# Kernel tuning notes

Measured on AMD Instinct MI355X. Metric: run time of the kernel, lower is better.

Reference implementation:

```python
import jax, jax.numpy as jnp
import numpy as np

# Fixed model constants from setParams()
TAU_W, TAU_N, TAU_R = 1.5e6, 6.0e5, 6.0e4
TAU_E, TAU_G, TAU_A = 2.5e4, 1.0e4, 1.0e4
F_W_MAX, F_N_MAX, F_R_MAX = 6.5, 5.0, 5.0
ALPHA_W, ALPHA_N, ALPHA_R = 0.5, 0.175, 0.13
BETA_W, BETA_R = -0.4, -0.9
GAMMA_E, GAMMA_G, GAMMA_A = 5.0, 4.0, 2.0
H_MAX, THETA_W = 1.0, 2.0
TAU_HW, TAU_HS = 3.483e7, 3.06e7
KAPPA = 1.5
A_RK = (0.5, 0.5, 1.0, 1.0)

T, B = 10000, 512


def setup_inputs() -> dict:
    key = jax.random.key(0)
    noise = 0.05 * jax.random.normal(key, (T, B), dtype=jnp.float32)
    return {
        "noise_input": noise,
        "g_RRe": jnp.float32(1.3),
        "g_RWe": jnp.float32(1.6),
        "g_WNi": jnp.float32(-2.0),
        "g_WRi": jnp.float32(-4.0),
        "g_NRi": jnp.float32(-1.3),
        "g_NWi": jnp.float32(-1.68),
    }


def _heaviside(x):
    # smooth heaviside: sigmoid with steepness 5
    return jax.nn.sigmoid(5.0 * x)


def reference(noise_input, g_RRe, g_RWe, g_WNi, g_WRi, g_NRi, g_NWi):
    b = noise_input.shape[1]
    dt = noise_input.dtype
    init = (
        jnp.full((b,), 6.0, dt),    # f_W
        jnp.full((b,), 1e-3, dt),   # f_N
        jnp.full((b,), 1e-3, dt),   # f_R
        jnp.full((b,), 0.9, dt),    # c_WXi
        jnp.full((b,), 1e-3, dt),   # c_NXi
        jnp.full((b,), 1e-3, dt),   # c_RXe
        jnp.full((b,), 0.5, dt),    # h
    )

    def step(state, noise):
        fW0, fN0, fR0, cW0, cN0, cR0, h0 = state
        # RK moment lists; index 0 is the step's initial value
        fW = [fW0]; fN = [fN0]; fR = [fR0]
        cW = [cW0]; cN = [cN0]; cR = [cR0]; hh = [h0]
        for n in range(4):
            a = A_RK[n]
            I_W = g_NWi * cN[n] + g_RWe * cR[n] + noise
            I_N = g_WNi * cW[n] + noise
            I_R = g_WRi * cW[n] + g_NRi * cN[n] + g_RRe * cR[n] + noise
            fW.append(fW[0] + a * (F_W_MAX * 0.5 * (1.0 + jnp.tanh((I_W - BETA_W) / ALPHA_W)) - fW[n]) / TAU_W)
            fN.append(fN[0] + a * (F_N_MAX * 0.5 * (1.0 + jnp.tanh((I_N + KAPPA * hh[n]) / ALPHA_N)) - fN[n]) / TAU_N)
            fR.append(fR[0] + a * (F_R_MAX * 0.5 * (1.0 + jnp.tanh((I_R - BETA_R) / ALPHA_R)) - fR[n]) / TAU_R)
            cW.append(cW[0] + a * (jnp.tanh(fW[n + 1] / GAMMA_E) - cW[n]) / TAU_E)
            cN.append(cN[0] + a * (jnp.tanh(fN[n + 1] / GAMMA_G) - cN[n]) / TAU_G)
            cR.append(cR[0] + a * (jnp.tanh(fR[n + 1] / GAMMA_A) - cR[n]) / TAU_A)
            hh.append(hh[0] + a * ((H_MAX - hh[n]) / TAU_HW * _heaviside(fW[n] - THETA_W)
                                   - hh[n] / TAU_HS * _heaviside(THETA_W - fW[n])))
        comb = lambda v: (-3.0 * v[0] + 2.0 * v[1] + 4.0 * v[2] + 2.0 * v[3] + v[4]) / 6.0
        new_state = tuple(comb(v) for v in (fW, fN, fR, cW, cN, cR, hh))
        return new_state, jnp.stack(new_state)  # [7, B]

    _, traj = jax.lax.scan(step, init, noise_input)
    return traj  # [T, 7, B]
```

## Files before the change

### kernel.cpp

```cpp
#include <hip/hip_runtime.h>

#define T_STEPS 10000
#define BATCH   512

__device__ __forceinline__ float fexp2(float x) {
#if __has_builtin(__builtin_amdgcn_exp2f)
  return __builtin_amdgcn_exp2f(x);
#else
  return exp2f(x);
#endif
}

__device__ __forceinline__ float frcp(float x) {
#if __has_builtin(__builtin_amdgcn_rcpf)
  return __builtin_amdgcn_rcpf(x);
#else
  return 1.0f / x;
#endif
}

#define PIN(x) asm volatile("" : "+v"(x))

template <int CTRL>
__device__ __forceinline__ float qperm(float v) {
  int i = __builtin_bit_cast(int, v);
#if __has_builtin(__builtin_amdgcn_mov_dpp)
  int r = __builtin_amdgcn_mov_dpp(i, CTRL, 0xF, 0xF, true);
#else
  int r = __builtin_amdgcn_ds_swizzle(i, 0x8000 | CTRL);
#endif
  return __builtin_bit_cast(float, r);
}

__global__ __launch_bounds__(64, 1)
void sleep_rk4_kernel(const float* __restrict__ noise,
                      const float* __restrict__ pgRRe,
                      const float* __restrict__ pgRWe,
                      const float* __restrict__ pgWNi,
                      const float* __restrict__ pgWRi,
                      const float* __restrict__ pgNRi,
                      const float* __restrict__ pgNWi,
                      float* __restrict__ out)
{
  __shared__ float shm[16 * 128];

  const int tid  = (int)(blockIdx.x * 64u + threadIdx.x);
  const int b    = tid >> 2;
  const int bl   = b & 15;
  const int role = tid & 3;

  const float g_RRe = *pgRRe, g_RWe = *pgRWe, g_WNi = *pgWNi;
  const float g_WRi = *pgWRi, g_NRi = *pgNRi, g_NWi = *pgNWi;

  const float L2E = 1.4426950408889634f;
  const float LN2 = 0.6931471805599453f;

  float W1, W2, W3, NSC, BB, qa, qb, pa, pb, cs, ia, ib;
  float f0, c0;
  bool role03;

  if (role == 0) {
    const float SC = 2.0f * L2E / 0.5f;
    W1 = SC * g_NWi; W2 = SC * g_RWe; W3 = 0.0f; NSC = SC; BB = SC * 0.4f;
    qa = -1.0f / 1.5e6f; qb = 6.5f / 1.5e6f; pa = 0.0f; pb = -6.5f / 1.5e6f;
    cs = 2.0f * L2E / 5.0f; ia = -1.0f / 2.5e4f; ib = 1.0f / 2.5e4f;
    f0 = 6.0f; c0 = 0.9f; role03 = true;
  } else if (role == 1) {
    const float SC = 2.0f * L2E / 0.175f;
    W1 = SC * g_WNi; W2 = SC * 1.5f; W3 = 0.0f; NSC = SC; BB = 0.0f;
    qa = -1.0f / 6.0e5f; qb = 5.0f / 6.0e5f; pa = 0.0f; pb = -5.0f / 6.0e5f;
    cs = 2.0f * L2E / 4.0f; ia = -1.0f / 1.0e4f; ib = 1.0f / 1.0e4f;
    f0 = 1.0e-3f; c0 = 1.0e-3f; role03 = false;
  } else if (role == 2) {
    const float SC = 2.0f * L2E / 0.13f;
    W1 = SC * g_WRi; W2 = SC * g_NRi; W3 = SC * g_RRe; NSC = SC; BB = SC * 0.9f;
    qa = -1.0f / 6.0e4f; qb = 5.0f / 6.0e4f; pa = 0.0f; pb = -5.0f / 6.0e4f;
    cs = 2.0f * L2E / 2.0f; ia = -1.0f / 1.0e4f; ib = 1.0f / 1.0e4f;
    f0 = 1.0e-3f; c0 = 1.0e-3f; role03 = false;
  } else {
    W1 = 0.0f; W2 = -5.0f * L2E; W3 = 0.0f; NSC = 0.0f; BB = 10.0f * L2E;
    qa = -1.0f / 3.06e7f; qb = 0.0f;
    pa = (1.0f / 3.06e7f - 1.0f / 3.483e7f);
    pb = 1.0f / 3.483e7f;
    cs = 0.0f; ia = 0.0f; ib = 0.0f;
    f0 = 0.5f; c0 = 0.0f; role03 = true;
  }

  const float AQAh = 0.5f * qa, AQA1 = qa;
  const float AIAh = 0.5f * ia, AIA1 = ia;
  const float IAC  = ia * cs;
  const float TIA  = 2.0f * ia;
  const float R6   = 0.16666666666666666f;

  float vF[4], vG[4];
  auto frun = [&](float f0b, float Gb, float* v) -> float {
    const float Chb = fmaf(0.5f, Gb, f0b), C1b = f0b + Gb;
    float s0 = f0b, acc = -3.0f * f0b;
    s0 = fmaf(AQAh, s0, Chb); v[0] = s0; acc = fmaf(2.0f, s0, acc);
    s0 = fmaf(AQAh, s0, Chb); v[1] = s0; acc = fmaf(4.0f, s0, acc);
    s0 = fmaf(AQA1, s0, C1b); v[2] = s0; acc = fmaf(2.0f, s0, acc);
    s0 = fmaf(AQA1, s0, C1b); v[3] = s0; acc = fmaf(1.0f, s0, acc);
    float q = acc * R6; q = fmaf(fmaf(q, -6.0f, acc), R6, q); return q;
  };
  const float KF = frun(1.0f, 0.0f, vF);
  const float KG = frun(0.0f, 1.0f, vG);

  auto crun = [&](const float* v, float c0b, float e1u, float vd1) -> float {
    const float E1h = IAC * e1u, E11 = 2.0f * IAC * e1u;
    const float Dh = c0b + 0.5f * vd1, D1 = c0b + vd1;
    float s1 = c0b, acc = -3.0f * c0b;
    s1 = fmaf(AIAh, s1, fmaf(E1h, v[0], Dh)); acc = fmaf(2.0f, s1, acc);
    s1 = fmaf(AIAh, s1, fmaf(E1h, v[1], Dh)); acc = fmaf(4.0f, s1, acc);
    s1 = fmaf(AIA1, s1, fmaf(E11, v[2], D1)); acc = fmaf(2.0f, s1, acc);
    s1 = fmaf(AIA1, s1, fmaf(E11, v[3], D1)); acc = fmaf(1.0f, s1, acc);
    float q = acc * R6; q = fmaf(fmaf(q, -6.0f, acc), R6, q); return q;
  };
  float z4[4] = {0.0f, 0.0f, 0.0f, 0.0f};
  const float KC  = crun(z4, 1.0f, 0.0f, 0.0f);
  const float LAf = crun(vF, 0.0f, 1.0f, 0.0f);
  const float LBf = crun(vG, 0.0f, 1.0f, 0.0f);
  const float KW  = crun(z4, 0.0f, 0.0f, 1.0f);

  const float KGi  = 1.0f / KG;
  const float LBfK = LBf * KGi;
  const float qbK  = qb * KG;

  float LAe, LBK, VDK, PK, tLAe, tLBK, tVDK, tPK;
  auto crefresh_compute = [&](float fcur) {
    const float zb = cs * fcur;
    const float ez = fexp2(zb);
    const float sc_ = frcp(1.0f + ez);
    const float t2 = fmaf(sc_, sc_, -sc_);
    const float e1 = LN2 * t2;
    const float vC = fmaf(-e1, zb, sc_);
    const float VD1 = fmaf(TIA, vC, ib);
    tLAe = LAf * e1; tLBK = LBfK * e1; tVDK = KW * VD1;
    tPK = fmaf(pa, fcur, pb) * KG;
  };
  crefresh_compute(f0);
  LAe = tLAe; LBK = tLBK; VDK = tVDK; PK = tPK;

  float dF = 0.0f, dC = 0.0f;
  float Gq0, Gq1, Gq2, Gq3, Gq4, Gq5, Gq6, Gq7;

  const int offA = role * 16 + bl;
  const int offB = (role + 4) * 16 + bl;

  int ldoff[7], goff[7];
  {
    const int L = (int)threadIdx.x;
    const int bb = (int)(blockIdx.x * 16u);
#pragma unroll
    for (int r = 0; r < 7; ++r) {
      const int F  = r * 64 + L;
      const int s_ = F / 28;
      const int u  = F % 28;
      const int rg = u >> 2;
      const int uu = u & 3;
      const int v  = (rg == 3) ? 6 : ((rg < 3) ? rg : rg - 1);
      ldoff[r] = s_ * 128 + u * 4;
      goff[r]  = s_ * 3584 + v * 512 + uu * 4 + bb;
    }
  }
  float* gflush = out;

  float nb0[16], nb1[16];
#pragma unroll
  for (int j = 0; j < 16; ++j) nb0[j] = noise[b + j * BATCH];

  {
    const float pubS = role03 ? f0 : c0;
    const float xAs = qperm<0x01>(c0);
    const float xBs = qperm<0x1E>(pubS);
    const float YB = fmaf(W1, xAs, fmaf(W2, xBs, fmaf(W3, c0, BB)));
    Gq0 = fmaf(PK, frcp(1.0f + fexp2(fmaf(NSC, nb0[0], YB))), qbK);
    Gq1 = fmaf(PK, frcp(1.0f + fexp2(fmaf(NSC, nb0[1], YB))), qbK);
    Gq2 = fmaf(PK, frcp(1.0f + fexp2(fmaf(NSC, nb0[2], YB))), qbK);
    Gq3 = fmaf(PK, frcp(1.0f + fexp2(fmaf(NSC, nb0[3], YB))), qbK);
    Gq4 = fmaf(PK, frcp(1.0f + fexp2(fmaf(NSC, nb0[4], YB))), qbK);
    Gq5 = fmaf(PK, frcp(1.0f + fexp2(fmaf(NSC, nb0[5], YB))), qbK);
    Gq6 = fmaf(PK, frcp(1.0f + fexp2(fmaf(NSC, nb0[6], YB))), qbK);
    Gq7 = fmaf(PK, frcp(1.0f + fexp2(fmaf(NSC, nb0[7], YB))), qbK);
  }

  auto GROUP8 = [&](int SJ, float n0, float n1, float n2, float n3,
                    float n4, float n5, float n6, float n7) {
    const float pubS = role03 ? f0 : c0;
    const float pubD = role03 ? dF : dC;
    const float xAs = qperm<0x01>(c0);
    const float xBs = qperm<0x1E>(pubS);
    const float xAd = qperm<0x01>(dC);
    const float xBd = qperm<0x1E>(pubD);
    float YB = fmaf(W3, c0, BB);
    float dY = W3 * dC;
    const float f1 = fmaf(KF, f0, Gq0);
    const float c1 = fmaf(KC, c0, fmaf(LAe, f0, fmaf(LBK, Gq0, VDK)));
    YB = fmaf(W2, xBs, YB);
    dY = fmaf(W2, xBd, dY);
    const float f2 = fmaf(KF, f1, Gq1);
    const float c2 = fmaf(KC, c1, fmaf(LAe, f1, fmaf(LBK, Gq1, VDK)));
    YB = fmaf(W1, xAs, YB);
    dY = fmaf(W1, xAd, dY);
    const float f3 = fmaf(KF, f2, Gq2);
    const float c3 = fmaf(KC, c2, fmaf(LAe, f2, fmaf(LBK, Gq2, VDK)));
    const float y0 = fmaf(NSC, n0, fmaf( 8.5f, dY, YB));
    const float y1 = fmaf(NSC, n1, fmaf( 9.5f, dY, YB));
    const float y2 = fmaf(NSC, n2, fmaf(10.5f, dY, YB));
    const float y3 = fmaf(NSC, n3, fmaf(11.5f, dY, YB));
    const float f4 = fmaf(KF, f3, Gq3);
    const float c4 = fmaf(KC, c3, fmaf(LAe, f3, fmaf(LBK, Gq3, VDK)));
    const float y4 = fmaf(NSC, n4, fmaf(12.5f, dY, YB));
    const float y5 = fmaf(NSC, n5, fmaf(13.5f, dY, YB));
    const float y6 = fmaf(NSC, n6, fmaf(14.5f, dY, YB));
    const float y7 = fmaf(NSC, n7, fmaf(15.5f, dY, YB));
    const float e0 = fexp2(y0);
    const float e1_ = fexp2(y1);
    const float f5 = fmaf(KF, f4, Gq4);
    const float c5 = fmaf(KC, c4, fmaf(LAe, f4, fmaf(LBK, Gq4, VDK)));
    const float e2 = fexp2(y2);
    const float e3 = fexp2(y3);
    const float f6 = fmaf(KF, f5, Gq5);
    const float c6 = fmaf(KC, c5, fmaf(LAe, f5, fmaf(LBK, Gq5, VDK)));
    const float e4 = fexp2(y4);
    const float e5 = fexp2(y5);
    const float f7 = fmaf(KF, f6, Gq6);
    const float c7 = fmaf(KC, c6, fmaf(LAe, f6, fmaf(LBK, Gq6, VDK)));
    const float e6 = fexp2(y6);
    const float e7 = fexp2(y7);
    const float f8 = fmaf(KF, f7, Gq7);
    const float c8 = fmaf(KC, c7, fmaf(LAe, f7, fmaf(LBK, Gq7, VDK)));
    const float r0 = frcp(1.0f + e0);
    const float r1 = frcp(1.0f + e1_);
    const float r2 = frcp(1.0f + e2);
    const float r3 = frcp(1.0f + e3);
    const float r4 = frcp(1.0f + e4);
    const float r5 = frcp(1.0f + e5);
    const float r6 = frcp(1.0f + e6);
    const float r7 = frcp(1.0f + e7);
    shm[(SJ + 0) * 128 + offA] = f1;  shm[(SJ + 0) * 128 + offB] = c1;
    shm[(SJ + 1) * 128 + offA] = f2;  shm[(SJ + 1) * 128 + offB] = c2;
    shm[(SJ + 2) * 128 + offA] = f3;  shm[(SJ + 2) * 128 + offB] = c3;
    shm[(SJ + 3) * 128 + offA] = f4;  shm[(SJ + 3) * 128 + offB] = c4;
    shm[(SJ + 4) * 128 + offA] = f5;  shm[(SJ + 4) * 128 + offB] = c5;
    shm[(SJ + 5) * 128 + offA] = f6;  shm[(SJ + 5) * 128 + offB] = c6;
    shm[(SJ + 6) * 128 + offA] = f7;  shm[(SJ + 6) * 128 + offB] = c7;
    shm[(SJ + 7) * 128 + offA] = f8;  shm[(SJ + 7) * 128 + offB] = c8;
    Gq0 = fmaf(PK, r0, qbK);
    Gq1 = fmaf(PK, r1, qbK);
    Gq2 = fmaf(PK, r2, qbK);
    Gq3 = fmaf(PK, r3, qbK);
    Gq4 = fmaf(PK, r4, qbK);
    Gq5 = fmaf(PK, r5, qbK);
    Gq6 = fmaf(PK, r6, qbK);
    Gq7 = fmaf(PK, r7, qbK);
    dF = f8 - f7; dC = c8 - c7;
    f0 = f8; c0 = c8;
  };

  int base = 0;

#define TBLOCK(nbC, nbN)                                                      \
  do {                                                                        \
    int tl = base + 16; if (tl > T_STEPS - 16) tl = T_STEPS - 16;             \
    const float* __restrict__ lp = noise + (size_t)tl * BATCH;                \
    _Pragma("unroll")                                                         \
    for (int j = 0; j < 16; ++j) nbN[j] = lp[b + j * BATCH];                  \
    _Pragma("unroll")                                                         \
    for (int j = 8; j < 16; ++j) PIN(nbC[j]);                                 \
    crefresh_compute(f0);                                                     \
    GROUP8(0, nbC[8], nbC[9], nbC[10], nbC[11],                               \
              nbC[12], nbC[13], nbC[14], nbC[15]);                            \
    LAe = tLAe; LBK = tLBK; VDK = tVDK; PK = tPK;                             \
    PIN(nbN[0]); PIN(nbN[1]); PIN(nbN[2]); PIN(nbN[3]);                       \
    PIN(nbN[4]); PIN(nbN[5]); PIN(nbN[6]); PIN(nbN[7]);                       \
    GROUP8(8, nbN[0], nbN[1], nbN[2], nbN[3],                                 \
              nbN[4], nbN[5], nbN[6], nbN[7]);                                \
    _Pragma("unroll")                                                         \
    for (int r = 0; r < 7; ++r) {                                             \
      const float4 vv = *(const float4*)&shm[ldoff[r]];                       \
      *(float4*)&gflush[goff[r]] = vv;                                        \
    }                                                                         \
    gflush += 16 * 3584;                                                      \
    base += 16;                                                               \
  } while (0)

  for (int kk = 0; kk < 312; ++kk) {
    TBLOCK(nb0, nb1);
    TBLOCK(nb1, nb0);
  }
  TBLOCK(nb0, nb1);
#undef TBLOCK
}

extern "C" void kernel_launch(void* const* d_in, const int* in_sizes, int n_in,
                              void* d_out, int out_size, void* d_ws, size_t ws_size,
                              hipStream_t stream) {
  const float* noise = (const float*)d_in[0];
  const float* gRRe  = (const float*)d_in[1];
  const float* gRWe  = (const float*)d_in[2];
  const float* gWNi  = (const float*)d_in[3];
  const float* gWRi  = (const float*)d_in[4];
  const float* gNRi  = (const float*)d_in[5];
  const float* gNWi  = (const float*)d_in[6];
  float* out = (float*)d_out;

  sleep_rk4_kernel<<<dim3((BATCH * 4) / 64), dim3(64), 0, stream>>>(
      noise, gRRe, gRWe, gWNi, gWRi, gNRi, gNWi, out);
}
```

Before: 471.9 us.

## Triple-buffer noise prefetch two blocks ahead and simplify output flush addressing

Noise loads now go into a rotation of three register buffers and are issued two 16-step blocks ahead instead of one, to hide more global-load latency behind the serial recurrence. The shared-to-global flush now uses a single advancing pointer with 8 strided float4 stores per lane, masked to 28 of every 32 lanes, replacing 7 precomputed offset pairs with div/mod layout. This lowers address-register pressure but adds 16 more live registers for noise and a divergent branch around the stores.

```diff
diff --git a/kernel.cpp b/kernel.cpp
--- a/kernel.cpp
+++ b/kernel.cpp
@@ -146,41 +146,35 @@
   const int offA = role * 16 + bl;
   const int offB = (role + 4) * 16 + bl;
 
-  int ldoff[7], goff[7];
+  const int  L        = (int)threadIdx.x;
+  const bool fluseful = ((L & 31) < 28);
+  float* gp;
   {
-    const int L = (int)threadIdx.x;
-    const int bb = (int)(blockIdx.x * 16u);
+    const int p  = L & 31;
+    const int rg = p >> 2;
+    const int v  = (rg == 3) ? 6 : ((rg < 3) ? rg : (rg > 6 ? 0 : rg - 1));
+    gp = out + (L >> 5) * 3584 + v * 512 + (p & 3) * 4 + (int)(blockIdx.x * 16u);
+  }
+
+  float nbA[16], nbB[16], nbCv[16];
 #pragma unroll
-    for (int r = 0; r < 7; ++r) {
-      const int F  = r * 64 + L;
-      const int s_ = F / 28;
-      const int u  = F % 28;
-      const int rg = u >> 2;
-      const int uu = u & 3;
-      const int v  = (rg == 3) ? 6 : ((rg < 3) ? rg : rg - 1);
-      ldoff[r] = s_ * 128 + u * 4;
-      goff[r]  = s_ * 3584 + v * 512 + uu * 4 + bb;
-    }
-  }
-  float* gflush = out;
-
-  float nb0[16], nb1[16];
+  for (int j = 0; j < 16; ++j) nbA[j] = noise[b + j * BATCH];
 #pragma unroll
-  for (int j = 0; j < 16; ++j) nb0[j] = noise[b + j * BATCH];
+  for (int j = 0; j < 16; ++j) nbB[j] = noise[b + (16 + j) * BATCH];
 
   {
     const float pubS = role03 ? f0 : c0;
     const float xAs = qperm<0x01>(c0);
     const float xBs = qperm<0x1E>(pubS);
     const float YB = fmaf(W1, xAs, fmaf(W2, xBs, fmaf(W3, c0, BB)));
-    Gq0 = fmaf(PK, frcp(1.0f + fexp2(fmaf(NSC, nb0[0], YB))), qbK);
-    Gq1 = fmaf(PK, frcp(1.0f + fexp2(fmaf(NSC, nb0[1], YB))), qbK);
-    Gq2 = fmaf(PK, frcp(1.0f + fexp2(fmaf(NSC, nb0[2], YB))), qbK);
-    Gq3 = fmaf(PK, frcp(1.0f + fexp2(fmaf(NSC, nb0[3], YB))), qbK);
-    Gq4 = fmaf(PK, frcp(1.0f + fexp2(fmaf(NSC, nb0[4], YB))), qbK);
-    Gq5 = fmaf(PK, frcp(1.0f + fexp2(fmaf(NSC, nb0[5], YB))), qbK);
-    Gq6 = fmaf(PK, frcp(1.0f + fexp2(fmaf(NSC, nb0[6], YB))), qbK);
-    Gq7 = fmaf(PK, frcp(1.0f + fexp2(fmaf(NSC, nb0[7], YB))), qbK);
+    Gq0 = fmaf(PK, frcp(1.0f + fexp2(fmaf(NSC, nbA[0], YB))), qbK);
+    Gq1 = fmaf(PK, frcp(1.0f + fexp2(fmaf(NSC, nbA[1], YB))), qbK);
+    Gq2 = fmaf(PK, frcp(1.0f + fexp2(fmaf(NSC, nbA[2], YB))), qbK);
+    Gq3 = fmaf(PK, frcp(1.0f + fexp2(fmaf(NSC, nbA[3], YB))), qbK);
+    Gq4 = fmaf(PK, frcp(1.0f + fexp2(fmaf(NSC, nbA[4], YB))), qbK);
+    Gq5 = fmaf(PK, frcp(1.0f + fexp2(fmaf(NSC, nbA[5], YB))), qbK);
+    Gq6 = fmaf(PK, frcp(1.0f + fexp2(fmaf(NSC, nbA[6], YB))), qbK);
+    Gq7 = fmaf(PK, frcp(1.0f + fexp2(fmaf(NSC, nbA[7], YB))), qbK);
   }
 
   auto GROUP8 = [&](int SJ, float n0, float n1, float n2, float n3,
@@ -259,36 +253,39 @@
 
   int base = 0;
 
-#define TBLOCK(nbC, nbN)                                                      \
+#define TBLOCK(nb1_, nb2_, nbL_)                                              \
   do {                                                                        \
-    int tl = base + 16; if (tl > T_STEPS - 16) tl = T_STEPS - 16;             \
+    int tl = base + 32; if (tl > T_STEPS - 16) tl = T_STEPS - 16;             \
     const float* __restrict__ lp = noise + (size_t)tl * BATCH;                \
     _Pragma("unroll")                                                         \
-    for (int j = 0; j < 16; ++j) nbN[j] = lp[b + j * BATCH];                  \
+    for (int j = 0; j < 16; ++j) nbL_[j] = lp[b + j * BATCH];                 \
     _Pragma("unroll")                                                         \
-    for (int j = 8; j < 16; ++j) PIN(nbC[j]);                                 \
+    for (int j = 8; j < 16; ++j) PIN(nb1_[j]);                                \
+    _Pragma("unroll")                                                         \
+    for (int j = 0; j < 8; ++j) PIN(nb2_[j]);                                 \
     crefresh_compute(f0);                                                     \
-    GROUP8(0, nbC[8], nbC[9], nbC[10], nbC[11],                               \
-              nbC[12], nbC[13], nbC[14], nbC[15]);                            \
+    GROUP8(0, nb1_[8], nb1_[9], nb1_[10], nb1_[11],                           \
+              nb1_[12], nb1_[13], nb1_[14], nb1_[15]);                        \
     LAe = tLAe; LBK = tLBK; VDK = tVDK; PK = tPK;                             \
-    PIN(nbN[0]); PIN(nbN[1]); PIN(nbN[2]); PIN(nbN[3]);                       \
-    PIN(nbN[4]); PIN(nbN[5]); PIN(nbN[6]); PIN(nbN[7]);                       \
-    GROUP8(8, nbN[0], nbN[1], nbN[2], nbN[3],                                 \
-              nbN[4], nbN[5], nbN[6], nbN[7]);                                \
-    _Pragma("unroll")                                                         \
-    for (int r = 0; r < 7; ++r) {                                             \
-      const float4 vv = *(const float4*)&shm[ldoff[r]];                       \
-      *(float4*)&gflush[goff[r]] = vv;                                        \
+    GROUP8(8, nb2_[0], nb2_[1], nb2_[2], nb2_[3],                             \
+              nb2_[4], nb2_[5], nb2_[6], nb2_[7]);                            \
+    if (fluseful) {                                                           \
+      _Pragma("unroll")                                                       \
+      for (int r = 0; r < 8; ++r) {                                           \
+        const float4 vv = *(const float4*)&shm[L * 4 + r * 256];              \
+        *(float4*)gp = vv;                                                    \
+        gp += 7168;                                                           \
+      }                                                                       \
     }                                                                         \
-    gflush += 16 * 3584;                                                      \
     base += 16;                                                               \
   } while (0)
 
-  for (int kk = 0; kk < 312; ++kk) {
-    TBLOCK(nb0, nb1);
-    TBLOCK(nb1, nb0);
+  for (int kk = 0; kk < 208; ++kk) {
+    TBLOCK(nbA, nbB, nbCv);
+    TBLOCK(nbB, nbCv, nbA);
+    TBLOCK(nbCv, nbA, nbB);
   }
-  TBLOCK(nb0, nb1);
+  TBLOCK(nbA, nbB, nbCv);
 #undef TBLOCK
 }
 
```

Measured after the change: 464.7 us, median of 2. Within noise of the previous version (-1.5%).
